# Kernel tuning notes

Hardware: AMD Instinct MI355X
Metric: run time of the kernel (lower is better)

## Reference

```python
import jax, jax.numpy as jnp
import numpy as np

N = 2_000_000
NODES = 16
FEAT = 19  # 9 (F) + 9 (cof F) + 1 (det F)


def setup_inputs() -> dict:
    key = jax.random.key(0)
    ks = jax.random.split(key, 9)
    # well-conditioned deformation gradients: F = I + 0.1*randn
    Fs = jnp.eye(3, dtype=jnp.float32) + 0.1 * jax.random.normal(ks[0], (N, 3, 3), dtype=jnp.float32)
    def glorot(k, shape):
        fan_in, fan_out = shape
        lim = np.sqrt(6.0 / (fan_in + fan_out)).astype(np.float32)
        return jax.random.uniform(k, shape, jnp.float32, -lim, lim)
    # layer 0: Dense(16, softplus); layers 1,2: Dense(16, softplus, non_neg kernel);
    # layer 3: Dense(1, linear, non_neg kernel). non_neg is a constraint applied
    # during training; we emulate by taking abs of the constrained kernels.
    W1 = glorot(ks[1], (FEAT, NODES)); b1 = jnp.zeros((NODES,), jnp.float32)
    W2 = jnp.abs(glorot(ks[2], (NODES, NODES))); b2 = jnp.zeros((NODES,), jnp.float32)
    W3 = jnp.abs(glorot(ks[3], (NODES, NODES))); b3 = jnp.zeros((NODES,), jnp.float32)
    W4 = jnp.abs(glorot(ks[4], (NODES, 1))); b4 = jnp.zeros((1,), jnp.float32)
    return {"Fs": Fs, "W1": W1, "b1": b1, "W2": W2, "b2": b2,
            "W3": W3, "b3": b3, "W4": W4, "b4": b4}


def _features(Fs):
    # det via closed-form 3x3 expansion (same value as tf.linalg.det)
    a, b, c = Fs[:, 0, 0], Fs[:, 0, 1], Fs[:, 0, 2]
    d, e, f = Fs[:, 1, 0], Fs[:, 1, 1], Fs[:, 1, 2]
    g, h, i = Fs[:, 2, 0], Fs[:, 2, 1], Fs[:, 2, 2]
    det = a * (e * i - f * h) - b * (d * i - f * g) + c * (d * h - e * g)
    # cof(F) = inv(F)^T * det  (original: transpose(inv(F)) @ diag(tile(det,3)))
    cof = jnp.swapaxes(jnp.linalg.inv(Fs), 1, 2) * det[:, None, None]
    # [N,19] = flat(F) ++ flat(cof) ++ det
    return jnp.concatenate([Fs.reshape(-1, 9), cof.reshape(-1, 9), det[:, None]], axis=1)


def reference(Fs, W1, b1, W2, b2, W3, b3, W4, b4):
    x = _features(Fs)
    x = jax.nn.softplus(x @ W1 + b1)
    x = jax.nn.softplus(x @ W2 + b2)
    x = jax.nn.softplus(x @ W3 + b3)
    return x @ W4 + b4  # [N,1]
```

## Files before the change

### kernel.cpp

```cpp
#include <hip/hip_runtime.h>
#include <hip/hip_fp16.h>
#include <math.h>

#define TPB 256
#define NODES 16
#define BLOCKS 2048

typedef float f32x4 __attribute__((ext_vector_type(4)));
typedef _Float16 half4 __attribute__((ext_vector_type(4)));
typedef _Float16 half8 __attribute__((ext_vector_type(8)));
typedef _Float16 h2 __attribute__((ext_vector_type(2)));

#define LOG2E 1.44269504088896340736f
#define LN2   0.69314718055994530942f

__device__ __forceinline__ _Float16 hx2(_Float16 x) {
    __half h = __builtin_bit_cast(__half, x);
    __half r = hexp2(h);
    return __builtin_bit_cast(_Float16, r);
}

__device__ __forceinline__ unsigned int sp2_pos(float v0, float v1) {
    h2 h = __builtin_bit_cast(h2, __builtin_amdgcn_cvt_pkrtz(v0, v1));
    h2 e = { hx2((_Float16)(-h[0])), hx2((_Float16)(-h[1])) };
    const h2 c3 = {(_Float16)0.154358f,  (_Float16)0.154358f};
    const h2 c2 = {(_Float16)-0.571177f, (_Float16)-0.571177f};
    const h2 c1 = {(_Float16)1.416467f,  (_Float16)1.416467f};
    h2 q = __builtin_elementwise_fma(e, __builtin_elementwise_fma(e, c3, c2), c1);
    h2 r = __builtin_elementwise_fma(e, q, h);
    return __builtin_bit_cast(unsigned int, r);
}
__device__ __forceinline__ unsigned int sp2_any(float v0, float v1) {
    h2 h = __builtin_bit_cast(h2, __builtin_amdgcn_cvt_pkrtz(v0, v1));
    const h2 z = {(_Float16)0.0f, (_Float16)0.0f};
    h2 m  = __builtin_elementwise_max(h, z);
    h2 nt = __builtin_elementwise_min(h, -h);
    h2 e = { hx2(nt[0]), hx2(nt[1]) };
    const h2 c3 = {(_Float16)0.154358f,  (_Float16)0.154358f};
    const h2 c2 = {(_Float16)-0.571177f, (_Float16)-0.571177f};
    const h2 c1 = {(_Float16)1.416467f,  (_Float16)1.416467f};
    h2 q = __builtin_elementwise_fma(e, __builtin_elementwise_fma(e, c3, c2), c1);
    h2 r = __builtin_elementwise_fma(e, q, m);
    return __builtin_bit_cast(unsigned int, r);
}
__device__ __forceinline__ unsigned int pk2(float a, float b) {
    return __builtin_bit_cast(unsigned int, __builtin_amdgcn_cvt_pkrtz(a, b));
}
__device__ __forceinline__ half4 h4(uint2 u) {
    return __builtin_bit_cast(half4, u);
}
__device__ __forceinline__ half8 h8(uint2 lo, uint2 hi) {
    uint4 u; u.x = lo.x; u.y = lo.y; u.z = hi.x; u.w = hi.y;
    return __builtin_bit_cast(half8, u);
}

__global__ __launch_bounds__(TPB, 4) void mlp_mfma_kernel(
    const float* __restrict__ Fs,
    const float* __restrict__ W1, const float* __restrict__ b1,
    const float* __restrict__ W2, const float* __restrict__ b2,
    const float* __restrict__ W3, const float* __restrict__ b3,
    const float* __restrict__ W4, const float* __restrict__ b4,
    float* __restrict__ out, int n, int iters)
{
    __shared__ uint2 lds[4][320];
    const int tid = threadIdx.x;
    const int l = tid & 63, w = tid >> 6;
    const int g = l >> 4, c = l & 15;

    half8 a1;
    half4 a2, a3, a4;
    f32x4 cb1, cb2, cb3;
    #pragma unroll
    for (int j = 0; j < 4; ++j) {
        a1[j]   = (_Float16)(W1[(4*g+j)*NODES + c] * LOG2E);
        a1[4+j] = (_Float16)((g == 0 && j < 3) ? W1[(16+j)*NODES + c] * LOG2E : 0.0f);
        a2[j]   = (_Float16)W2[(4*g+j)*NODES + c];
        a3[j]   = (_Float16)W3[(4*g+j)*NODES + c];
        a4[j]   = (_Float16)(W4[4*g+j] * LN2);
    }
    const float b4s = b4[0];
    #pragma unroll
    for (int i = 0; i < 4; ++i) {
        cb1[i] = b1[4*g+i] * LOG2E;
        cb2[i] = b2[4*g+i] * LOG2E;
        cb3[i] = b3[4*g+i] * LOG2E;
    }
    const f32x4 zero4 = {0.0f, 0.0f, 0.0f, 0.0f};

    uint2* basep = &lds[w][0];
    const long long s0 = ((long long)blockIdx.x * 4 + w) * (64LL * iters);
    if (s0 >= n) return;

    float fr[9];
    {
        long long sE = s0 + l; if (sE > n - 1) sE = n - 1;
        const float* fp = Fs + sE * 9;
        #pragma unroll
        for (int q = 0; q < 9; ++q) fr[q] = fp[q];
    }

    for (int it = 0; it < iters; ++it) {
        long long ws = s0 + (long long)it * 64;
        if (ws >= n) break;

        float a = fr[0], b = fr[1], cc = fr[2];
        float d = fr[3], e = fr[4], f5 = fr[5];
        float g7 = fr[6], h7 = fr[7], i8 = fr[8];

        const bool havenext = (it + 1 < iters) && (ws + 64 < n);
        if (havenext) {
            long long sE = ws + 64 + l; if (sE > n - 1) sE = n - 1;
            const float* fp = Fs + sE * 9;
            #pragma unroll
            for (int q = 0; q < 9; ++q) fr[q] = fp[q];
        }

        float C00 = e * i8 - f5 * h7;
        float C01 = f5 * g7 - d * i8;
        float C02 = d * h7 - e * g7;
        float det = fmaf(a, C00, fmaf(b, C01, cc * C02));
        float C10 = cc * h7 - b * i8;
        float C11 = a * i8 - cc * g7;
        float C12 = b * g7 - a * h7;
        float C20 = b * f5 - cc * e;
        float C21 = cc * d - a * f5;
        float C22 = a * e - b * d;

        {
            uint2 v;
            v.x = pk2(a,   b);   v.y = pk2(cc,  d);   basep[l*5 + 0] = v;
            v.x = pk2(e,   f5);  v.y = pk2(g7,  h7);  basep[l*5 + 1] = v;
            v.x = pk2(i8,  C00); v.y = pk2(C01, C02); basep[l*5 + 2] = v;
            v.x = pk2(C10, C11); v.y = pk2(C12, C20); basep[l*5 + 3] = v;
            v.x = pk2(C21, C22); v.y = pk2(det, 0.0f); basep[l*5 + 4] = v;
        }
        asm volatile("s_waitcnt lgkmcnt(0)" ::: "memory");

        uint2 rlo0 = basep[(16*0 + c)*5 + g];
        uint2 rlo1 = basep[(16*1 + c)*5 + g];
        uint2 rlo2 = basep[(16*2 + c)*5 + g];
        uint2 rlo3 = basep[(16*3 + c)*5 + g];
        uint2 rhi0 = basep[(16*0 + c)*5 + 4];
        uint2 rhi1 = basep[(16*1 + c)*5 + 4];
        uint2 rhi2 = basep[(16*2 + c)*5 + 4];
        uint2 rhi3 = basep[(16*3 + c)*5 + 4];

        f32x4 t10 = __builtin_amdgcn_mfma_f32_16x16x32_f16(a1, h8(rlo0, rhi0), cb1, 0, 0, 0);
        f32x4 t11 = __builtin_amdgcn_mfma_f32_16x16x32_f16(a1, h8(rlo1, rhi1), cb1, 0, 0, 0);
        f32x4 t12 = __builtin_amdgcn_mfma_f32_16x16x32_f16(a1, h8(rlo2, rhi2), cb1, 0, 0, 0);
        f32x4 t13 = __builtin_amdgcn_mfma_f32_16x16x32_f16(a1, h8(rlo3, rhi3), cb1, 0, 0, 0);

        uint2 u0, u1, u2, u3;
        u0.x = sp2_any(t10[0], t10[1]); u0.y = sp2_any(t10[2], t10[3]);
        u1.x = sp2_any(t11[0], t11[1]); u1.y = sp2_any(t11[2], t11[3]);
        u2.x = sp2_any(t12[0], t12[1]); u2.y = sp2_any(t12[2], t12[3]);
        u3.x = sp2_any(t13[0], t13[1]); u3.y = sp2_any(t13[2], t13[3]);

        f32x4 d20 = __builtin_amdgcn_mfma_f32_16x16x16f16(a2, h4(u0), cb2, 0, 0, 0);
        f32x4 d21 = __builtin_amdgcn_mfma_f32_16x16x16f16(a2, h4(u1), cb2, 0, 0, 0);
        f32x4 d22 = __builtin_amdgcn_mfma_f32_16x16x16f16(a2, h4(u2), cb2, 0, 0, 0);
        f32x4 d23 = __builtin_amdgcn_mfma_f32_16x16x16f16(a2, h4(u3), cb2, 0, 0, 0);

        u0.x = sp2_pos(d20[0], d20[1]); u0.y = sp2_pos(d20[2], d20[3]);
        u1.x = sp2_pos(d21[0], d21[1]); u1.y = sp2_pos(d21[2], d21[3]);
        u2.x = sp2_pos(d22[0], d22[1]); u2.y = sp2_pos(d22[2], d22[3]);
        u3.x = sp2_pos(d23[0], d23[1]); u3.y = sp2_pos(d23[2], d23[3]);

        f32x4 d30 = __builtin_amdgcn_mfma_f32_16x16x16f16(a3, h4(u0), cb3, 0, 0, 0);
        f32x4 d31 = __builtin_amdgcn_mfma_f32_16x16x16f16(a3, h4(u1), cb3, 0, 0, 0);
        f32x4 d32 = __builtin_amdgcn_mfma_f32_16x16x16f16(a3, h4(u2), cb3, 0, 0, 0);
        f32x4 d33 = __builtin_amdgcn_mfma_f32_16x16x16f16(a3, h4(u3), cb3, 0, 0, 0);

        u0.x = sp2_pos(d30[0], d30[1]); u0.y = sp2_pos(d30[2], d30[3]);
        u1.x = sp2_pos(d31[0], d31[1]); u1.y = sp2_pos(d31[2], d31[3]);
        u2.x = sp2_pos(d32[0], d32[1]); u2.y = sp2_pos(d32[2], d32[3]);
        u3.x = sp2_pos(d33[0], d33[1]); u3.y = sp2_pos(d33[2], d33[3]);

        f32x4 d40 = __builtin_amdgcn_mfma_f32_16x16x16f16(a4, h4(u0), zero4, 0, 0, 0);
        f32x4 d41 = __builtin_amdgcn_mfma_f32_16x16x16f16(a4, h4(u1), zero4, 0, 0, 0);
        f32x4 d42 = __builtin_amdgcn_mfma_f32_16x16x16f16(a4, h4(u2), zero4, 0, 0, 0);
        f32x4 d43 = __builtin_amdgcn_mfma_f32_16x16x16f16(a4, h4(u3), zero4, 0, 0, 0);

        float yo = (g == 0) ? d40[0] : ((g == 1) ? d41[0] : ((g == 2) ? d42[0] : d43[0]));
        yo += b4s;
        if (ws + l < n) out[ws + l] = yo;
    }
}

extern "C" void kernel_launch(void* const* d_in, const int* in_sizes, int n_in,
                              void* d_out, int out_size, void* d_ws, size_t ws_size,
                              hipStream_t stream) {
    const float* Fs = (const float*)d_in[0];
    const float* W1 = (const float*)d_in[1];
    const float* b1 = (const float*)d_in[2];
    const float* W2 = (const float*)d_in[3];
    const float* b2 = (const float*)d_in[4];
    const float* W3 = (const float*)d_in[5];
    const float* b3 = (const float*)d_in[6];
    const float* W4 = (const float*)d_in[7];
    const float* b4 = (const float*)d_in[8];
    float* out = (float*)d_out;

    int n = in_sizes[0] / 9;
    int waves = (n + 63) / 64;
    int iters = (waves + BLOCKS * 4 - 1) / (BLOCKS * 4);
    mlp_mfma_kernel<<<BLOCKS, TPB, 0, stream>>>(Fs, W1, b1, W2, b2, W3, b3, W4, b4,
                                                out, n, iters);
}
```

Measured before the change: 28.07 us.

## Stage input tiles via direct global-to-LDS 16-byte loads with double buffering

Replaces the per-lane strided 9-float register loads of each deformation gradient with coalesced 16-byte global_load_lds transfers of the wave's contiguous 64x9 float tile into a double-buffered LDS region. Each lane then reads its nine values from LDS. The aim is fewer, wider, coalesced memory transactions and no register pressure from prefetched values. The cost is extra LDS per block (which may lower occupancy), extra LDS reads, and a full vmcnt(0) wait each iteration. That wait also waits on the output store, and the 9*64 tile size assumes 16-byte alignment of the tile start (s*9/4 truncation).

New measurement: 30.15 us. +7.4%, slower.

```diff
diff --git a/kernel.cpp b/kernel.cpp
--- a/kernel.cpp
+++ b/kernel.cpp
@@ -53,6 +53,12 @@
     uint4 u; u.x = lo.x; u.y = lo.y; u.z = hi.x; u.w = hi.y;
     return __builtin_bit_cast(half8, u);
 }
+__device__ __forceinline__ void gl2lds(const float* g, void* l) {
+    __builtin_amdgcn_global_load_lds(
+        (const __attribute__((address_space(1))) unsigned int*)g,
+        (__attribute__((address_space(3))) unsigned int*)l,
+        16, 0, 0);
+}
 
 __global__ __launch_bounds__(TPB, 4) void mlp_mfma_kernel(
     const float* __restrict__ Fs,
@@ -62,7 +68,8 @@
     const float* __restrict__ W4, const float* __restrict__ b4,
     float* __restrict__ out, int n, int iters)
 {
-    __shared__ uint2 lds[4][320];
+    __shared__ uint2 feats[4][320];
+    __shared__ float raw[4][2][768];
     const int tid = threadIdx.x;
     const int l = tid & 63, w = tid >> 6;
     const int g = l >> 4, c = l & 15;
@@ -87,33 +94,44 @@
     }
     const f32x4 zero4 = {0.0f, 0.0f, 0.0f, 0.0f};
 
-    uint2* basep = &lds[w][0];
+    uint2* basep = &feats[w][0];
     const long long s0 = ((long long)blockIdx.x * 4 + w) * (64LL * iters);
     if (s0 >= n) return;
 
-    float fr[9];
-    {
-        long long sE = s0 + l; if (sE > n - 1) sE = n - 1;
-        const float* fp = Fs + sE * 9;
-        #pragma unroll
-        for (int q = 0; q < 9; ++q) fr[q] = fp[q];
-    }
+    const long long maxf4 = (long long)n * 9 / 4 - 1;
+
+    #define STAGE(S, BUF)                                                        \
+        do {                                                                     \
+            long long f4b = (S) * 9LL / 4LL;                                     \
+            _Pragma("unroll")                                                    \
+            for (int k2 = 0; k2 < 3; ++k2) {                                     \
+                long long idx = f4b + l + 64 * k2;                               \
+                if (idx > maxf4) idx = maxf4;                                    \
+                gl2lds(Fs + idx * 4, &raw[w][BUF][k2 * 256]);                    \
+            }                                                                    \
+        } while (0)
+
+    STAGE(s0, 0);
 
     for (int it = 0; it < iters; ++it) {
         long long ws = s0 + (long long)it * 64;
         if (ws >= n) break;
-
-        float a = fr[0], b = fr[1], cc = fr[2];
-        float d = fr[3], e = fr[4], f5 = fr[5];
-        float g7 = fr[6], h7 = fr[7], i8 = fr[8];
+        const int cur = it & 1;
+
+        asm volatile("s_waitcnt vmcnt(0)" ::: "memory");
+
+        float a  = raw[w][cur][l*9 + 0];
+        float b  = raw[w][cur][l*9 + 1];
+        float cc = raw[w][cur][l*9 + 2];
+        float d  = raw[w][cur][l*9 + 3];
+        float e  = raw[w][cur][l*9 + 4];
+        float f5 = raw[w][cur][l*9 + 5];
+        float g7 = raw[w][cur][l*9 + 6];
+        float h7 = raw[w][cur][l*9 + 7];
+        float i8 = raw[w][cur][l*9 + 8];
 
         const bool havenext = (it + 1 < iters) && (ws + 64 < n);
-        if (havenext) {
-            long long sE = ws + 64 + l; if (sE > n - 1) sE = n - 1;
-            const float* fp = Fs + sE * 9;
-            #pragma unroll
-            for (int q = 0; q < 9; ++q) fr[q] = fp[q];
-        }
+        if (havenext) STAGE(ws + 64, cur ^ 1);
 
         float C00 = e * i8 - f5 * h7;
         float C01 = f5 * g7 - d * i8;
@@ -185,6 +203,7 @@
         yo += b4s;
         if (ws + l < n) out[ws + l] = yo;
     }
+    #undef STAGE
 }
 
 extern "C" void kernel_launch(void* const* d_in, const int* in_sizes, int n_in,
```
